# Optimization experiments

Hardware: AMD Instinct MI355X
Metric: run time of the kernel (lower is better)

## Reference

```python
import jax, jax.numpy as jnp
import numpy as np

INPUT, HIDDEN, CLASSES = 4096, 4096, 1000


def setup_inputs() -> dict:
    key = jax.random.key(0)
    kx, kw1, kb1, kw2, kb2 = jax.random.split(key, 5)
    return {
        "x": jax.random.normal(kx, (8192, INPUT), dtype=jnp.float32),
        "fc1_weight": jax.random.normal(kw1, (HIDDEN, INPUT), dtype=jnp.float32),
        "fc1_bias": jax.random.normal(kb1, (HIDDEN,), dtype=jnp.float32),
        "fc2_weight": jax.random.normal(kw2, (CLASSES, HIDDEN), dtype=jnp.float32),
        "fc2_bias": jax.random.normal(kb2, (CLASSES,), dtype=jnp.float32),
    }


def reference(x, fc1_weight, fc1_bias, fc2_weight, fc2_bias):
    # x: [B, INPUT] (module flattens; already flat here)
    hidden = jnp.einsum("bi,hi->bh", x, fc1_weight) + fc1_bias  # [B, H]
    activated = jax.nn.relu(hidden)
    logits = jnp.einsum("bh,ch->bc", activated, fc2_weight) + fc2_bias  # [B, C]
    return jax.nn.softmax(logits, axis=-1)
```

## Files before the change

### kernel.cpp

```cpp
#include <hip/hip_runtime.h>
#include <hip/hip_fp16.h>
#include <stdint.h>

typedef __attribute__((ext_vector_type(8)))  _Float16 f16x8;
typedef __attribute__((ext_vector_type(4)))  _Float16 f16x4;
typedef __attribute__((ext_vector_type(4)))  float    f32x4;
typedef __attribute__((ext_vector_type(16))) float    f32x16;

__device__ __forceinline__ void split4(const f32x4 v, f16x4 &h, f16x4 &l) {
    #pragma unroll
    for (int i = 0; i < 4; ++i) {
        float a = v[i];
        _Float16 hh = (_Float16)a;
        h[i] = hh;
        l[i] = (_Float16)(a - (float)hh);
    }
}

__global__ __launch_bounds__(256)
void split_rows(const float* __restrict__ src, _Float16* __restrict__ h,
                _Float16* __restrict__ l, int srcRows, long long total4)
{
    const long long stride = (long long)gridDim.x * blockDim.x;
    for (long long i = (long long)blockIdx.x * blockDim.x + threadIdx.x; i < total4; i += stride) {
        const long long e = i << 2;
        const int row = (int)(e >> 12);
        f16x4 hv = {}, lv = {};
        if (row < srcRows) {
            f32x4 v = *(const f32x4*)(src + e);
            split4(v, hv, lv);
        }
        *(f16x4*)(h + e) = hv;
        *(f16x4*)(l + e) = lv;
    }
}


#define BARRIER() __builtin_amdgcn_s_barrier()
#define SB0()     __builtin_amdgcn_sched_barrier(0)
#define MFMA32    __builtin_amdgcn_mfma_f32_32x32x16_f16

template<int N> __device__ __forceinline__ void VMCNT() {
    asm volatile("s_waitcnt vmcnt(%0)" :: "n"(N) : "memory");
    __builtin_amdgcn_sched_barrier(0);
}

__device__ __forceinline__ void gload16(const _Float16* g, _Float16* l) {
    __builtin_amdgcn_global_load_lds(
        (const __attribute__((address_space(1))) void*)g,
        (__attribute__((address_space(3))) void*)l, 16, 0, 0);
}

template<int MI, bool SPLITOUT, bool CHUNKSWZ>
__global__ __launch_bounds__(512, 2)
void gemm3_v7(const _Float16* __restrict__ Agh, const _Float16* __restrict__ Agl,
              const _Float16* __restrict__ Bgh, const _Float16* __restrict__ Bgl,
              const float* __restrict__ bias,
              _Float16* __restrict__ Oh, _Float16* __restrict__ Ol,
              float* __restrict__ Of, int ldo, int Nstore,
              int K, int nBN)
{
    extern __shared__ _Float16 lds[];
    constexpr int WROWS = MI * 16;
    constexpr int BM    = MI * 32;
    constexpr int MB    = MI / 2;
    constexpr int CHA   = MI * 2;
    constexpr int PW    = (2*CHA + 32) / 8;
    constexpr int H1    = PW - CHA/8;
    constexpr int H2    = CHA / 8;
    constexpr int ALO   = CHA * 512;
    constexpr int BHO   = 2 * CHA * 512;
    constexpr int BUFS  = 2*CHA*512 + 16384;

    const int tid  = threadIdx.x;
    const int lane = tid & 63;
    const int wave = tid >> 6;
    const int wm  = wave >> 2;
    const int wn  = wave & 3;
    const int l31 = lane & 31;
    const int lhi = lane >> 5;

    int bm, bn;
    const int orig = blockIdx.x;
    if (CHUNKSWZ) {
        bm = ((orig & 7) << 2) | ((orig >> 3) & 3);
        bn = orig >> 5;
    } else {
        const int cpx  = gridDim.x >> 3;
        const int swzb = (orig & 7) * cpx + (orig >> 3);
        bn = swzb % nBN;
        bm = swzb / nBN;
    }
    const int m0 = bm * BM;
    const int n0 = bn * 256;

    const _Float16* gptr[8];
    int loff[8];
    #pragma unroll
    for (int i = 0; i < PW; ++i) {
        int p, q;
        if (i < H2 || i >= H1) {
            const bool hi = (i >= H1);
            const int  s  = hi ? (i - H1) : i;
            const int  j  = wave * H2 + s;
            p = j / (CHA / 2);
            const int v   = j % (CHA / 2);
            const int wmq = v / (MI / 2);
            const int wi  = v % (MI / 2);
            q = wmq * MI + (hi ? MI / 2 : 0) + wi;
        } else {
            q = (i - H2) + (wave & 3) * 4;
            p = 2 + (wave >> 2);
        }
        const int row = q*16 + (lane >> 2);
        const int gc  = (lane & 3) ^ ((row >> 1) & 3);
        const _Float16* plane = (p == 0) ? Agh : (p == 1) ? Agl : (p == 2) ? Bgh : Bgl;
        const size_t grow = (size_t)((p < 2) ? m0 : n0) + row;
        gptr[i] = plane + grow * (size_t)K + gc * 8;
        loff[i] = ((p < 2) ? p * ALO : BHO + (p - 2) * 8192) + q * 512;
    }

    const int kxor = (l31 >> 1) & 3;
    int aoff[MB][2], boff[2][2];
    #pragma unroll
    for (int mb = 0; mb < MB; ++mb)
        #pragma unroll
        for (int kh = 0; kh < 2; ++kh)
            aoff[mb][kh] = (wm*WROWS + mb*32 + l31)*32 + ((lhi*2 + kh) ^ kxor)*8;
    #pragma unroll
    for (int nb2 = 0; nb2 < 2; ++nb2)
        #pragma unroll
        for (int kh = 0; kh < 2; ++kh)
            boff[nb2][kh] = BHO + (wn*64 + nb2*32 + l31)*32 + ((lhi*2 + kh) ^ kxor)*8;

    f32x16 acc[MB][2] = {};

    #pragma unroll
    for (int i = 0; i < PW; ++i) { gload16(gptr[i], &lds[loff[i]]); gptr[i] += 32; }
    VMCNT<0>(); BARRIER(); SB0();

    const int NT = K >> 5;
    int bb = 0;
    for (int t = 0; t < NT; ++t) {
        const int nbuf = BUFS - bb;
        if (t < NT - 1) {
            #pragma unroll
            for (int i = 0; i < PW; ++i) { gload16(gptr[i], &lds[nbuf + loff[i]]); gptr[i] += 32; }
        }
        SB0();
        f16x8 bh[2][2], bl[2][2];
        #pragma unroll
        for (int nb2 = 0; nb2 < 2; ++nb2)
            #pragma unroll
            for (int kh = 0; kh < 2; ++kh) {
                bh[nb2][kh] = *(const f16x8*)&lds[bb + boff[nb2][kh]];
                bl[nb2][kh] = *(const f16x8*)&lds[bb + 8192 + boff[nb2][kh]];
            }
        #pragma unroll
        for (int kh = 0; kh < 2; ++kh) {
            #pragma unroll
            for (int mb = 0; mb < MB; ++mb) {
                const f16x8 ah = *(const f16x8*)&lds[bb + aoff[mb][kh]];
                const f16x8 al = *(const f16x8*)&lds[bb + ALO + aoff[mb][kh]];
                #pragma unroll
                for (int n2 = 0; n2 < 2; ++n2) {
                    acc[mb][n2] = MFMA32(ah, bh[n2][kh], acc[mb][n2], 0, 0, 0);
                    acc[mb][n2] = MFMA32(ah, bl[n2][kh], acc[mb][n2], 0, 0, 0);
                    acc[mb][n2] = MFMA32(al, bh[n2][kh], acc[mb][n2], 0, 0, 0);
                }
            }
        }
        VMCNT<0>(); BARRIER(); SB0();
        bb = nbuf;
    }

    #pragma unroll
    for (int nb2 = 0; nb2 < 2; ++nb2) {
        const int n = n0 + wn*64 + nb2*32 + l31;
        if (!SPLITOUT && n >= Nstore) continue;
        const float bv = bias[n];
        #pragma unroll
        for (int mb = 0; mb < MB; ++mb) {
            #pragma unroll
            for (int r = 0; r < 16; ++r) {
                const int m = m0 + wm*WROWS + mb*32 + (r & 3) + 8*(r >> 2) + 4*lhi;
                float v = acc[mb][nb2][r] + bv;
                if (SPLITOUT) {
                    v = fmaxf(v, 0.f);
                    const _Float16 hh = (_Float16)v;
                    Oh[(size_t)m * ldo + n] = hh;
                    Ol[(size_t)m * ldo + n] = (_Float16)(v - (float)hh);
                } else {
                    Of[(size_t)m * ldo + n] = v;
                }
            }
        }
    }
}

#define TILE_M 128
#define TILE_N 128
#define TILE_K 32
#define LDSK   40

template<bool RELU, bool NGUARD>
__global__ __launch_bounds__(256, 2)
void gemm_split3(const float* __restrict__ A, const float* __restrict__ B,
                 const float* __restrict__ bias, float* __restrict__ C,
                 int K, int ldc, int Nreal)
{
    __shared__ _Float16 Ah[TILE_M][LDSK];
    __shared__ _Float16 Al[TILE_M][LDSK];
    __shared__ _Float16 Bh[TILE_N][LDSK];
    __shared__ _Float16 Bl[TILE_N][LDSK];

    const int tid  = threadIdx.x;
    const int lane = tid & 63;
    const int wave = tid >> 6;
    const int wr   = wave >> 1;
    const int wc   = wave & 1;
    const int m0   = blockIdx.x * TILE_M;
    const int n0   = blockIdx.y * TILE_N;
    const int srow = tid >> 3;
    const int scol = (tid & 7) << 2;
    const int fr = lane & 15;
    const int fg = lane >> 4;

    f32x4 acc[4][4] = {};

    for (int kt = 0; kt < K; kt += TILE_K) {
        __syncthreads();
        #pragma unroll
        for (int p = 0; p < 4; ++p) {
            const int row = srow + p * 32;
            f32x4 v = *(const f32x4*)(A + (size_t)(m0 + row) * K + kt + scol);
            f16x4 hv, lv;
            split4(v, hv, lv);
            *(f16x4*)&Ah[row][scol] = hv;
            *(f16x4*)&Al[row][scol] = lv;
        }
        #pragma unroll
        for (int p = 0; p < 4; ++p) {
            const int row = srow + p * 32;
            f32x4 v = {0.f, 0.f, 0.f, 0.f};
            if (!NGUARD || (n0 + row) < Nreal)
                v = *(const f32x4*)(B + (size_t)(n0 + row) * K + kt + scol);
            f16x4 hv, lv;
            split4(v, hv, lv);
            *(f16x4*)&Bh[row][scol] = hv;
            *(f16x4*)&Bl[row][scol] = lv;
        }
        __syncthreads();

        f16x8 ah[4], al[4];
        #pragma unroll
        for (int mi = 0; mi < 4; ++mi) {
            const int r = wr * 64 + mi * 16 + fr;
            ah[mi] = *(const f16x8*)&Ah[r][fg * 8];
            al[mi] = *(const f16x8*)&Al[r][fg * 8];
        }
        #pragma unroll
        for (int ni = 0; ni < 4; ++ni) {
            const int r = wc * 64 + ni * 16 + fr;
            const f16x8 bh = *(const f16x8*)&Bh[r][fg * 8];
            const f16x8 bl = *(const f16x8*)&Bl[r][fg * 8];
            #pragma unroll
            for (int mi = 0; mi < 4; ++mi) {
                acc[mi][ni] = __builtin_amdgcn_mfma_f32_16x16x32_f16(ah[mi], bh, acc[mi][ni], 0, 0, 0);
                acc[mi][ni] = __builtin_amdgcn_mfma_f32_16x16x32_f16(ah[mi], bl, acc[mi][ni], 0, 0, 0);
                acc[mi][ni] = __builtin_amdgcn_mfma_f32_16x16x32_f16(al[mi], bh, acc[mi][ni], 0, 0, 0);
            }
        }
    }

    #pragma unroll
    for (int ni = 0; ni < 4; ++ni) {
        const int n = n0 + wc * 64 + ni * 16 + fr;
        if (NGUARD && n >= Nreal) continue;
        const float bv = bias[n];
        #pragma unroll
        for (int mi = 0; mi < 4; ++mi) {
            #pragma unroll
            for (int j = 0; j < 4; ++j) {
                const int m = m0 + wr * 64 + mi * 16 + fg * 4 + j;
                float val = acc[mi][ni][j] + bv;
                if (RELU) val = fmaxf(val, 0.f);
                C[(size_t)m * ldc + n] = val;
            }
        }
    }
}

__global__ __launch_bounds__(256)
void softmax_rows(float* __restrict__ out, int rows, int cols)
{
    const int lane = threadIdx.x & 63;
    const int row  = blockIdx.x * 4 + (threadIdx.x >> 6);
    if (row >= rows) return;
    float* p = out + (size_t)row * cols;

    float v[16];
    float mx = -3.4e38f;
    #pragma unroll
    for (int j = 0; j < 16; ++j) {
        const int c = lane + j * 64;
        v[j] = (c < cols) ? p[c] : -3.4e38f;
        mx = fmaxf(mx, v[j]);
    }
    #pragma unroll
    for (int off = 32; off > 0; off >>= 1)
        mx = fmaxf(mx, __shfl_xor(mx, off));

    float s = 0.f;
    #pragma unroll
    for (int j = 0; j < 16; ++j) {
        const int c = lane + j * 64;
        const float e = (c < cols) ? __expf(v[j] - mx) : 0.f;
        v[j] = e;
        s += e;
    }
    #pragma unroll
    for (int off = 32; off > 0; off >>= 1)
        s += __shfl_xor(s, off);

    const float inv = 1.f / s;
    #pragma unroll
    for (int j = 0; j < 16; ++j) {
        const int c = lane + j * 64;
        if (c < cols) p[c] = v[j] * inv;
    }
}

extern "C" void kernel_launch(void* const* d_in, const int* in_sizes, int n_in,
                              void* d_out, int out_size, void* d_ws, size_t ws_size,
                              hipStream_t stream)
{
    const float* x  = (const float*)d_in[0];
    const float* w1 = (const float*)d_in[1];
    const float* b1 = (const float*)d_in[2];
    const float* w2 = (const float*)d_in[3];
    const float* b2 = (const float*)d_in[4];
    float* out = (float*)d_out;

    const size_t SZ_X  = (size_t)8192 * 4096 * 2;
    const size_t SZ_W1 = (size_t)4096 * 4096 * 2;
    const size_t SZ_W2 = (size_t)1024 * 4096 * 2;

    size_t off = 0;
    auto take = [&](size_t b) { size_t o = off; off += (b + 255) & ~(size_t)255; return o; };
    const size_t o_xh  = take(SZ_X),  o_xl  = take(SZ_X);
    const size_t o_w1h = take(SZ_W1), o_w1l = take(SZ_W1);
    const size_t o_w2h = take(SZ_W2), o_w2l = take(SZ_W2);
    const size_t o_ah  = take(SZ_X),  o_al  = take(SZ_X);
    const size_t need = off;

    bool attr_ok =
        (hipFuncSetAttribute((const void*)gemm3_v7<8, true, true>,
                             hipFuncAttributeMaxDynamicSharedMemorySize, 131072) == hipSuccess) &&
        (hipFuncSetAttribute((const void*)gemm3_v7<4, false, false>,
                             hipFuncAttributeMaxDynamicSharedMemorySize, 131072) == hipSuccess);

    const dim3 blk256(256, 1, 1), blk512(512, 1, 1);

    if (attr_ok && ws_size >= need) {
        char* w = (char*)d_ws;
        _Float16 *xh  = (_Float16*)(w + o_xh),  *xl  = (_Float16*)(w + o_xl);
        _Float16 *w1h = (_Float16*)(w + o_w1h), *w1l = (_Float16*)(w + o_w1l);
        _Float16 *w2h = (_Float16*)(w + o_w2h), *w2l = (_Float16*)(w + o_w2l);
        _Float16 *ath = (_Float16*)(w + o_ah),  *atl = (_Float16*)(w + o_al);

        hipLaunchKernelGGL(split_rows, dim3(2048), blk256, 0, stream, x,  xh,  xl,  8192, (long long)8192 * 1024);
        hipLaunchKernelGGL(split_rows, dim3(2048), blk256, 0, stream, w1, w1h, w1l, 4096, (long long)4096 * 1024);
        hipLaunchKernelGGL(split_rows, dim3(1024), blk256, 0, stream, w2, w2h, w2l, 1000, (long long)1024 * 1024);

        hipLaunchKernelGGL((gemm3_v7<8, true, true>), dim3(512), blk512, 131072, stream,
                           xh, xl, w1h, w1l, b1, ath, atl, (float*)nullptr, 4096, 4096, 4096, 16);
        hipLaunchKernelGGL((gemm3_v7<4, false, false>), dim3(256), blk512, 98304, stream,
                           ath, atl, w2h, w2l, b2, (_Float16*)nullptr, (_Float16*)nullptr,
                           out, 1000, 1000, 4096, 4);
        hipLaunchKernelGGL(softmax_rows, dim3(2048), blk256, 0, stream, out, 8192, 1000);
    } else {
        float* act = (float*)d_ws;
        hipLaunchKernelGGL((gemm_split3<true, false>), dim3(64, 32), blk256, 0, stream,
                           x, w1, b1, act, 4096, 4096, 4096);
        hipLaunchKernelGGL((gemm_split3<false, true>), dim3(64, 8), blk256, 0, stream,
                           act, w2, b2, out, 4096, 1000, 1000);
        hipLaunchKernelGGL(softmax_rows, dim3(2048), blk256, 0, stream, out, 8192, 1000);
    }
}
```

Measured before the change: 1.060 ms.

## Switch GEMM to 16x16x32 MFMA with interleaved LDS prefetch scheduling

Replaces the 32x32x16 MFMA tiling with 16x16x32 fragments, so each lane reads one swizzled 8-wide K chunk per fragment. Adds software prefetch of the next A fragment and sched_group_barrier hints to interleave LDS reads and global loads with MFMAs. Peels the last K iteration so the loop has no conditional prefetch. The aim is to hide LDS latency and improve MFMA issue density. The trade-off is more accumulator registers and more MFMA instructions, which may hurt occupancy at 2 blocks per CU.

```diff
diff --git a/kernel.cpp b/kernel.cpp
--- a/kernel.cpp
+++ b/kernel.cpp
@@ -5,7 +5,6 @@
 typedef __attribute__((ext_vector_type(8)))  _Float16 f16x8;
 typedef __attribute__((ext_vector_type(4)))  _Float16 f16x4;
 typedef __attribute__((ext_vector_type(4)))  float    f32x4;
-typedef __attribute__((ext_vector_type(16))) float    f32x16;
 
 __device__ __forceinline__ void split4(const f32x4 v, f16x4 &h, f16x4 &l) {
     #pragma unroll
@@ -38,7 +37,8 @@
 
 #define BARRIER() __builtin_amdgcn_s_barrier()
 #define SB0()     __builtin_amdgcn_sched_barrier(0)
-#define MFMA32    __builtin_amdgcn_mfma_f32_32x32x16_f16
+#define MFMA16    __builtin_amdgcn_mfma_f32_16x16x32_f16
+#define SGB       __builtin_amdgcn_sched_group_barrier
 
 template<int N> __device__ __forceinline__ void VMCNT() {
     asm volatile("s_waitcnt vmcnt(%0)" :: "n"(N) : "memory");
@@ -53,7 +53,7 @@
 
 template<int MI, bool SPLITOUT, bool CHUNKSWZ>
 __global__ __launch_bounds__(512, 2)
-void gemm3_v7(const _Float16* __restrict__ Agh, const _Float16* __restrict__ Agl,
+void gemm3_v8(const _Float16* __restrict__ Agh, const _Float16* __restrict__ Agl,
               const _Float16* __restrict__ Bgh, const _Float16* __restrict__ Bgl,
               const float* __restrict__ bias,
               _Float16* __restrict__ Oh, _Float16* __restrict__ Ol,
@@ -63,7 +63,6 @@
     extern __shared__ _Float16 lds[];
     constexpr int WROWS = MI * 16;
     constexpr int BM    = MI * 32;
-    constexpr int MB    = MI / 2;
     constexpr int CHA   = MI * 2;
     constexpr int PW    = (2*CHA + 32) / 8;
     constexpr int H1    = PW - CHA/8;
@@ -75,10 +74,10 @@
     const int tid  = threadIdx.x;
     const int lane = tid & 63;
     const int wave = tid >> 6;
-    const int wm  = wave >> 2;
-    const int wn  = wave & 3;
-    const int l31 = lane & 31;
-    const int lhi = lane >> 5;
+    const int wm = wave >> 2;
+    const int wn = wave & 3;
+    const int fr = lane & 15;
+    const int fg = lane >> 4;
 
     int bm, bn;
     const int orig = blockIdx.x;
@@ -120,20 +119,14 @@
         loff[i] = ((p < 2) ? p * ALO : BHO + (p - 2) * 8192) + q * 512;
     }
 
-    const int kxor = (l31 >> 1) & 3;
-    int aoff[MB][2], boff[2][2];
-    #pragma unroll
-    for (int mb = 0; mb < MB; ++mb)
-        #pragma unroll
-        for (int kh = 0; kh < 2; ++kh)
-            aoff[mb][kh] = (wm*WROWS + mb*32 + l31)*32 + ((lhi*2 + kh) ^ kxor)*8;
-    #pragma unroll
-    for (int nb2 = 0; nb2 < 2; ++nb2)
-        #pragma unroll
-        for (int kh = 0; kh < 2; ++kh)
-            boff[nb2][kh] = BHO + (wn*64 + nb2*32 + l31)*32 + ((lhi*2 + kh) ^ kxor)*8;
-
-    f32x16 acc[MB][2] = {};
+    const int swz8 = (fg ^ ((fr >> 1) & 3)) * 8;
+    int aoff[MI], boff[4];
+    #pragma unroll
+    for (int mi = 0; mi < MI; ++mi) aoff[mi] = (wm*WROWS + mi*16 + fr)*32 + swz8;
+    #pragma unroll
+    for (int ni = 0; ni < 4; ++ni)  boff[ni] = BHO + (wn*64 + ni*16 + fr)*32 + swz8;
+
+    f32x4 acc[MI][4] = {};
 
     #pragma unroll
     for (int i = 0; i < PW; ++i) { gload16(gptr[i], &lds[loff[i]]); gptr[i] += 32; }
@@ -141,50 +134,80 @@
 
     const int NT = K >> 5;
     int bb = 0;
-    for (int t = 0; t < NT; ++t) {
+    for (int t = 0; t < NT - 1; ++t) {
         const int nbuf = BUFS - bb;
-        if (t < NT - 1) {
+        #pragma unroll
+        for (int i = 0; i < PW; ++i) { gload16(gptr[i], &lds[nbuf + loff[i]]); gptr[i] += 32; }
+        f16x8 bh[4], bl[4];
+        #pragma unroll
+        for (int ni = 0; ni < 4; ++ni) {
+            bh[ni] = *(const f16x8*)&lds[bb + boff[ni]];
+            bl[ni] = *(const f16x8*)&lds[bb + 8192 + boff[ni]];
+        }
+        f16x8 ah = *(const f16x8*)&lds[bb + aoff[0]];
+        f16x8 al = *(const f16x8*)&lds[bb + ALO + aoff[0]];
+        SGB(0x010, PW, 0);
+        SGB(0x100, 10, 0);
+        #pragma unroll
+        for (int mi = 0; mi < MI; ++mi) {
+            f16x8 ahn, aln;
+            if (mi < MI - 1) {
+                ahn = *(const f16x8*)&lds[bb + aoff[mi + 1]];
+                aln = *(const f16x8*)&lds[bb + ALO + aoff[mi + 1]];
+            }
             #pragma unroll
-            for (int i = 0; i < PW; ++i) { gload16(gptr[i], &lds[nbuf + loff[i]]); gptr[i] += 32; }
-        }
-        SB0();
-        f16x8 bh[2][2], bl[2][2];
-        #pragma unroll
-        for (int nb2 = 0; nb2 < 2; ++nb2)
-            #pragma unroll
-            for (int kh = 0; kh < 2; ++kh) {
-                bh[nb2][kh] = *(const f16x8*)&lds[bb + boff[nb2][kh]];
-                bl[nb2][kh] = *(const f16x8*)&lds[bb + 8192 + boff[nb2][kh]];
-            }
-        #pragma unroll
-        for (int kh = 0; kh < 2; ++kh) {
-            #pragma unroll
-            for (int mb = 0; mb < MB; ++mb) {
-                const f16x8 ah = *(const f16x8*)&lds[bb + aoff[mb][kh]];
-                const f16x8 al = *(const f16x8*)&lds[bb + ALO + aoff[mb][kh]];
-                #pragma unroll
-                for (int n2 = 0; n2 < 2; ++n2) {
-                    acc[mb][n2] = MFMA32(ah, bh[n2][kh], acc[mb][n2], 0, 0, 0);
-                    acc[mb][n2] = MFMA32(ah, bl[n2][kh], acc[mb][n2], 0, 0, 0);
-                    acc[mb][n2] = MFMA32(al, bh[n2][kh], acc[mb][n2], 0, 0, 0);
-                }
-            }
+            for (int ni = 0; ni < 4; ++ni) {
+                acc[mi][ni] = MFMA16(ah, bh[ni], acc[mi][ni], 0, 0, 0);
+                acc[mi][ni] = MFMA16(ah, bl[ni], acc[mi][ni], 0, 0, 0);
+                acc[mi][ni] = MFMA16(al, bh[ni], acc[mi][ni], 0, 0, 0);
+            }
+            if (mi < MI - 1) SGB(0x100, 2, 0);
+            SGB(0x008, 12, 0);
+            if (mi < MI - 1) { ah = ahn; al = aln; }
         }
         VMCNT<0>(); BARRIER(); SB0();
         bb = nbuf;
     }
-
-    #pragma unroll
-    for (int nb2 = 0; nb2 < 2; ++nb2) {
-        const int n = n0 + wn*64 + nb2*32 + l31;
+    {
+        f16x8 bh[4], bl[4];
+        #pragma unroll
+        for (int ni = 0; ni < 4; ++ni) {
+            bh[ni] = *(const f16x8*)&lds[bb + boff[ni]];
+            bl[ni] = *(const f16x8*)&lds[bb + 8192 + boff[ni]];
+        }
+        f16x8 ah = *(const f16x8*)&lds[bb + aoff[0]];
+        f16x8 al = *(const f16x8*)&lds[bb + ALO + aoff[0]];
+        SGB(0x100, 10, 0);
+        #pragma unroll
+        for (int mi = 0; mi < MI; ++mi) {
+            f16x8 ahn, aln;
+            if (mi < MI - 1) {
+                ahn = *(const f16x8*)&lds[bb + aoff[mi + 1]];
+                aln = *(const f16x8*)&lds[bb + ALO + aoff[mi + 1]];
+            }
+            #pragma unroll
+            for (int ni = 0; ni < 4; ++ni) {
+                acc[mi][ni] = MFMA16(ah, bh[ni], acc[mi][ni], 0, 0, 0);
+                acc[mi][ni] = MFMA16(ah, bl[ni], acc[mi][ni], 0, 0, 0);
+                acc[mi][ni] = MFMA16(al, bh[ni], acc[mi][ni], 0, 0, 0);
+            }
+            if (mi < MI - 1) SGB(0x100, 2, 0);
+            SGB(0x008, 12, 0);
+            if (mi < MI - 1) { ah = ahn; al = aln; }
+        }
+    }
+
+    #pragma unroll
+    for (int ni = 0; ni < 4; ++ni) {
+        const int n = n0 + wn*64 + ni*16 + fr;
         if (!SPLITOUT && n >= Nstore) continue;
         const float bv = bias[n];
         #pragma unroll
-        for (int mb = 0; mb < MB; ++mb) {
+        for (int mi = 0; mi < MI; ++mi) {
             #pragma unroll
-            for (int r = 0; r < 16; ++r) {
-                const int m = m0 + wm*WROWS + mb*32 + (r & 3) + 8*(r >> 2) + 4*lhi;
-                float v = acc[mb][nb2][r] + bv;
+            for (int j = 0; j < 4; ++j) {
+                const int m = m0 + wm*WROWS + mi*16 + fg*4 + j;
+                float v = acc[mi][ni][j] + bv;
                 if (SPLITOUT) {
                     v = fmaxf(v, 0.f);
                     const _Float16 hh = (_Float16)v;
@@ -355,9 +378,9 @@
     const size_t need = off;
 
     bool attr_ok =
-        (hipFuncSetAttribute((const void*)gemm3_v7<8, true, true>,
+        (hipFuncSetAttribute((const void*)gemm3_v8<8, true, true>,
                              hipFuncAttributeMaxDynamicSharedMemorySize, 131072) == hipSuccess) &&
-        (hipFuncSetAttribute((const void*)gemm3_v7<4, false, false>,
+        (hipFuncSetAttribute((const void*)gemm3_v8<4, false, false>,
                              hipFuncAttributeMaxDynamicSharedMemorySize, 131072) == hipSuccess);
 
     const dim3 blk256(256, 1, 1), blk512(512, 1, 1);
@@ -373,9 +396,9 @@
         hipLaunchKernelGGL(split_rows, dim3(2048), blk256, 0, stream, w1, w1h, w1l, 4096, (long long)4096 * 1024);
         hipLaunchKernelGGL(split_rows, dim3(1024), blk256, 0, stream, w2, w2h, w2l, 1000, (long long)1024 * 1024);
 
-        hipLaunchKernelGGL((gemm3_v7<8, true, true>), dim3(512), blk512, 131072, stream,
+        hipLaunchKernelGGL((gemm3_v8<8, true, true>), dim3(512), blk512, 131072, stream,
                            xh, xl, w1h, w1l, b1, ath, atl, (float*)nullptr, 4096, 4096, 4096, 16);
-        hipLaunchKernelGGL((gemm3_v7<4, false, false>), dim3(256), blk512, 98304, stream,
+        hipLaunchKernelGGL((gemm3_v8<4, false, false>), dim3(256), blk512, 98304, stream,
                            ath, atl, w2h, w2l, b2, (_Float16*)nullptr, (_Float16*)nullptr,
                            out, 1000, 1000, 4096, 4);
         hipLaunchKernelGGL(softmax_rows, dim3(2048), blk256, 0, stream, out, 8192, 1000);
```

New measurement: 943.7 us. 1.12x faster.
